# Optimization experiments

Hardware: AMD Instinct MI355X
Metric: run time of the kernel (lower is better)

The kernel has to match this reference:

```python
import jax, jax.numpy as jnp
import numpy as np

# Faithful JAX version of ROIMask_To_Img / paste_mask_in_image (Mask R-CNN paste):
# per box: (mask+1)/2, zero-pad by 1, expand box by (M+2)/M, truncate to int,
# bilinear-resize (align_corners=False, edge-clamped) to the box extent, and
# overwrite-paste into the image canvas; final canvas is mapped to [-1, 1].
# Instead of per-box dynamic-size interpolate + slice assignment, we evaluate the
# bilinear resample densely over the full image grid and mask to the box region
# (same math, jit-compatible, single fused gather-resize-scatter).


def _edge_coords(s, size):
    # torch bilinear align_corners=False with edge clamping
    s = jnp.clip(s, 0.0, size - 1.0)
    i0 = jnp.floor(s)
    t = s - i0
    i0 = i0.astype(jnp.int32)
    i1 = jnp.minimum(i0 + 1, size - 1)
    return i0, i1, t


def _paste_step(im, mask, box):
    # im: [H, W] canvas; mask: [M, M] in [-1,1]; box: [4] float (x0, y0, x1, y1)
    H, W = im.shape
    M = mask.shape[-1]
    Mp = M + 2  # padded mask size
    m = jnp.pad((mask + 1.0) * 0.5, 1)  # expand_masks(padding=1) -> [Mp, Mp]
    scale = (M + 2.0) / M
    w_half = (box[2] - box[0]) * (0.5 * scale)
    h_half = (box[3] - box[1]) * (0.5 * scale)
    x_c = (box[2] + box[0]) * 0.5
    y_c = (box[3] + box[1]) * 0.5
    # expand_boxes then .to(int32) (truncation toward zero, like torch)
    b = jnp.trunc(jnp.stack([x_c - w_half, y_c - h_half,
                             x_c + w_half, y_c + h_half])).astype(jnp.int32)
    w = jnp.maximum(b[2] - b[0] + 1, 1).astype(jnp.float32)
    h = jnp.maximum(b[3] - b[1] + 1, 1).astype(jnp.float32)
    px = jnp.arange(H)
    py = jnp.arange(W)
    # source coords in padded-mask space (align_corners=False)
    sx = (px - b[0] + 0.5) * (Mp / w) - 0.5  # [H]
    sy = (py - b[1] + 0.5) * (Mp / h) - 0.5  # [W]
    x0, x1, tx = _edge_coords(sx, Mp)
    y0, y1, ty = _edge_coords(sy, Mp)
    # separable bilinear: mix rows first ([H, Mp]), then columns ([H, W])
    rowmix = m[x0] * (1.0 - tx)[:, None] + m[x1] * tx[:, None]
    val = rowmix[:, y0] * (1.0 - ty)[None, :] + rowmix[:, y1] * ty[None, :]
    # paste region (overwrite semantics, clipped to the image)
    vx = (px >= b[0]) & (px <= b[2])
    vy = (py >= b[1]) & (py <= b[3])
    return jnp.where(vx[:, None] & vy[None, :], val, im)


def setup_inputs() -> dict:
    key = jax.random.key(0)
    B, N, M, H, W = 32, 16, 28, 1024, 1024
    k1, k2, k3, k4 = jax.random.split(key, 4)
    masks = jax.random.uniform(k1, (B, N, 1, M, M), jnp.float32, -1.0, 1.0)
    # valid boxes inside the image: corner + extent
    p0 = jax.random.uniform(k2, (B, N, 2), jnp.float32, 0.0, H - 64.0)
    ext = jax.random.uniform(k3, (B, N, 2), jnp.float32, 16.0, 200.0)
    p1 = jnp.minimum(p0 + ext, H - 2.0)
    rects = jnp.concatenate([p0, p1], axis=-1)  # [B, N, 4] = (x0, y0, x1, y1)
    instance_mask = jnp.zeros((B, 1, H, W), jnp.float32)
    return {"masks": masks, "rects": rects, "instance_mask": instance_mask}


def reference(masks, rects, instance_mask):
    # masks: [B, N, 1, M, M]; rects: [B, N, 4]; instance_mask: [B, 1, H, W]
    H, W = instance_mask.shape[-2], instance_mask.shape[-1]

    def per_image(masks_b, rects_b):
        im0 = jnp.zeros((H, W), jnp.float32)
        def step(im, xs):
            m, bx = xs
            return _paste_step(im, m, bx), None
        im, _ = jax.lax.scan(step, im0, (masks_b[:, 0], rects_b))
        return im

    im = jax.vmap(per_image)(masks, rects)  # [B, H, W]
    return im[:, None, :, :] * 2.0 - 1.0
```

## Files before the change

### kernel.cpp

```cpp
#include <hip/hip_runtime.h>

constexpr int Bc = 32;
constexpr int Nc = 16;
constexpr int Mc = 28;
constexpr int MPc = 30;
constexpr int Hc = 1024;
constexpr int Wc = 1024;

__global__ __launch_bounds__(256)
void paste_masks_kernel(const float* __restrict__ masks,
                        const float* __restrict__ rects,
                        float* __restrict__ out)
{
    const int bid = blockIdx.x;
    const int b   = bid >> 10;
    const int row = bid & (Hc - 1);
    const int tid = threadIdx.x;

    __shared__ int   s_r0[Nc], s_r2[Nc];
    __shared__ int   s_c1[Nc], s_c3[Nc];
    __shared__ float s_sxs[Nc], s_sys[Nc];
    __shared__ int   s_list[Nc];
    __shared__ int   s_cnt;
    __shared__ float s_rowmix[Nc][MPc];

    if (tid < Nc) {
        const float* r = rects + (b * Nc + tid) * 4;
        const float x0 = r[0], y0 = r[1], x1 = r[2], y1 = r[3];
        const float hs = 0.5357142857142857f;
        const float w_half = (x1 - x0) * hs;
        const float h_half = (y1 - y0) * hs;
        const float xc = (x1 + x0) * 0.5f;
        const float yc = (y1 + y0) * 0.5f;
        const int ib0 = (int)truncf(xc - w_half);
        const int ib1 = (int)truncf(yc - h_half);
        const int ib2 = (int)truncf(xc + w_half);
        const int ib3 = (int)truncf(yc + h_half);
        s_r0[tid] = ib0; s_r2[tid] = ib2;
        s_c1[tid] = ib1; s_c3[tid] = ib3;
        const float w = fmaxf((float)(ib2 - ib0 + 1), 1.0f);
        const float h = fmaxf((float)(ib3 - ib1 + 1), 1.0f);
        s_sxs[tid] = (float)MPc / w;
        s_sys[tid] = (float)MPc / h;
    }
    __syncthreads();

    if (tid == 0) {
        int c = 0;
        for (int n = Nc - 1; n >= 0; --n)
            if (row >= s_r0[n] && row <= s_r2[n]) s_list[c++] = n;
        s_cnt = c;
    }
    __syncthreads();
    const int cnt = s_cnt;

    if (cnt > 0) {
        for (int idx = tid; idx < cnt * MPc; idx += 256) {
            const int k = idx / MPc;
            const int j = idx - k * MPc;
            const int n = s_list[k];
            float sx = ((float)(row - s_r0[n]) + 0.5f) * s_sxs[n] - 0.5f;
            sx = fminf(fmaxf(sx, 0.0f), (float)(MPc - 1));
            const int   i0 = (int)floorf(sx);
            const float tx = sx - (float)i0;
            const int   i1 = min(i0 + 1, MPc - 1);
            const float* mp = masks + (size_t)(b * Nc + n) * (Mc * Mc);
            float m0 = 0.0f, m1 = 0.0f;
            if (i0 >= 1 && i0 <= Mc && j >= 1 && j <= Mc)
                m0 = (mp[(i0 - 1) * Mc + (j - 1)] + 1.0f) * 0.5f;
            if (i1 >= 1 && i1 <= Mc && j >= 1 && j <= Mc)
                m1 = (mp[(i1 - 1) * Mc + (j - 1)] + 1.0f) * 0.5f;
            s_rowmix[k][j] = m0 * (1.0f - tx) + m1 * tx;
        }
        __syncthreads();
    }

    const int col0 = tid * 4;
    float4 v;
    float* vp = (float*)&v;
    #pragma unroll
    for (int c = 0; c < 4; ++c) {
        const int col = col0 + c;
        float val = -1.0f;
        for (int k = 0; k < cnt; ++k) {
            const int n = s_list[k];
            if (col >= s_c1[n] && col <= s_c3[n]) {
                float sy = ((float)(col - s_c1[n]) + 0.5f) * s_sys[n] - 0.5f;
                sy = fminf(fmaxf(sy, 0.0f), (float)(MPc - 1));
                const int   j0 = (int)floorf(sy);
                const float ty = sy - (float)j0;
                const int   j1 = min(j0 + 1, MPc - 1);
                const float s = s_rowmix[k][j0] * (1.0f - ty) + s_rowmix[k][j1] * ty;
                val = s * 2.0f - 1.0f;
                break;
            }
        }
        vp[c] = val;
    }

    float4* op = (float4*)(out + (size_t)bid * Wc) + tid;
    *op = v;
}

extern "C" void kernel_launch(void* const* d_in, const int* in_sizes, int n_in,
                              void* d_out, int out_size, void* d_ws, size_t ws_size,
                              hipStream_t stream) {
    const float* masks = (const float*)d_in[0];
    const float* rects = (const float*)d_in[1];
    float* out = (float*)d_out;

    const int grid = Bc * Hc;
    paste_masks_kernel<<<grid, 256, 0, stream>>>(masks, rects, out);
}
```

Baseline: 256.9 us.

## Process 8 rows per block with box bitmasks and direct global bilinear gathers

Each block now covers 8 output rows instead of one. This spreads the per-block rect setup across more output and cuts the grid by 8x. The serial per-row box list and the shared rowmix staging are replaced by per-row and per-column box bitmasks, and the topmost box is found with a count-leading-zeros. The bilinear sample now does four global (cache-served) mask loads per covered pixel instead of two shared reads, trading extra memory gathers for fewer barriers and no serial thread-0 loop.

```diff
diff --git a/kernel.cpp b/kernel.cpp
--- a/kernel.cpp
+++ b/kernel.cpp
@@ -1,28 +1,28 @@
 #include <hip/hip_runtime.h>
 
-constexpr int Bc = 32;
-constexpr int Nc = 16;
-constexpr int Mc = 28;
+constexpr int Bc  = 32;
+constexpr int Nc  = 16;
+constexpr int Mc  = 28;
 constexpr int MPc = 30;
-constexpr int Hc = 1024;
-constexpr int Wc = 1024;
+constexpr int Hc  = 1024;
+constexpr int Wc  = 1024;
+constexpr int ROWS = 8;
 
 __global__ __launch_bounds__(256)
 void paste_masks_kernel(const float* __restrict__ masks,
                         const float* __restrict__ rects,
                         float* __restrict__ out)
 {
-    const int bid = blockIdx.x;
-    const int b   = bid >> 10;
-    const int row = bid & (Hc - 1);
-    const int tid = threadIdx.x;
+    const int tiles_per_img = Hc / ROWS;
+    const int bid  = blockIdx.x;
+    const int b    = bid / tiles_per_img;
+    const int row0 = (bid - b * tiles_per_img) * ROWS;
+    const int tid  = threadIdx.x;
 
-    __shared__ int   s_r0[Nc], s_r2[Nc];
-    __shared__ int   s_c1[Nc], s_c3[Nc];
-    __shared__ float s_sxs[Nc], s_sys[Nc];
-    __shared__ int   s_list[Nc];
-    __shared__ int   s_cnt;
-    __shared__ float s_rowmix[Nc][MPc];
+    __shared__ int      s_r0[Nc], s_r2[Nc];
+    __shared__ int      s_c1[Nc], s_c3[Nc];
+    __shared__ float    s_sxs[Nc], s_sys[Nc];
+    __shared__ unsigned s_rowmask[ROWS];
 
     if (tid < Nc) {
         const float* r = rects + (b * Nc + tid) * 4;
@@ -45,61 +45,72 @@
     }
     __syncthreads();
 
-    if (tid == 0) {
-        int c = 0;
-        for (int n = Nc - 1; n >= 0; --n)
-            if (row >= s_r0[n] && row <= s_r2[n]) s_list[c++] = n;
-        s_cnt = c;
-    }
-    __syncthreads();
-    const int cnt = s_cnt;
-
-    if (cnt > 0) {
-        for (int idx = tid; idx < cnt * MPc; idx += 256) {
-            const int k = idx / MPc;
-            const int j = idx - k * MPc;
-            const int n = s_list[k];
-            float sx = ((float)(row - s_r0[n]) + 0.5f) * s_sxs[n] - 0.5f;
-            sx = fminf(fmaxf(sx, 0.0f), (float)(MPc - 1));
-            const int   i0 = (int)floorf(sx);
-            const float tx = sx - (float)i0;
-            const int   i1 = min(i0 + 1, MPc - 1);
-            const float* mp = masks + (size_t)(b * Nc + n) * (Mc * Mc);
-            float m0 = 0.0f, m1 = 0.0f;
-            if (i0 >= 1 && i0 <= Mc && j >= 1 && j <= Mc)
-                m0 = (mp[(i0 - 1) * Mc + (j - 1)] + 1.0f) * 0.5f;
-            if (i1 >= 1 && i1 <= Mc && j >= 1 && j <= Mc)
-                m1 = (mp[(i1 - 1) * Mc + (j - 1)] + 1.0f) * 0.5f;
-            s_rowmix[k][j] = m0 * (1.0f - tx) + m1 * tx;
-        }
-        __syncthreads();
+    if (tid < ROWS) {
+        const int row = row0 + tid;
+        unsigned m = 0;
+        #pragma unroll
+        for (int n = 0; n < Nc; ++n)
+            if (row >= s_r0[n] && row <= s_r2[n]) m |= (1u << n);
+        s_rowmask[tid] = m;
     }
 
     const int col0 = tid * 4;
-    float4 v;
-    float* vp = (float*)&v;
+    unsigned cmask[4];
     #pragma unroll
     for (int c = 0; c < 4; ++c) {
         const int col = col0 + c;
-        float val = -1.0f;
-        for (int k = 0; k < cnt; ++k) {
-            const int n = s_list[k];
-            if (col >= s_c1[n] && col <= s_c3[n]) {
+        unsigned m = 0;
+        #pragma unroll
+        for (int n = 0; n < Nc; ++n)
+            if (col >= s_c1[n] && col <= s_c3[n]) m |= (1u << n);
+        cmask[c] = m;
+    }
+    __syncthreads();
+
+    const float* mbase = masks + (size_t)b * (Nc * Mc * Mc);
+    float* orow = out + (size_t)b * Hc * Wc + (size_t)row0 * Wc;
+
+    for (int rr = 0; rr < ROWS; ++rr) {
+        const int row = row0 + rr;
+        const unsigned rm = s_rowmask[rr];
+        float4 v;
+        float* vp = (float*)&v;
+        #pragma unroll
+        for (int c = 0; c < 4; ++c) {
+            const unsigned m = cmask[c] & rm;
+            float val = -1.0f;
+            if (m) {
+                const int n = 31 - __clz((int)m);
+                float sx = ((float)(row - s_r0[n]) + 0.5f) * s_sxs[n] - 0.5f;
+                sx = fminf(fmaxf(sx, 0.0f), (float)(MPc - 1));
+                const int   i0 = (int)floorf(sx);
+                const float tx = sx - (float)i0;
+                const int   i1 = min(i0 + 1, MPc - 1);
+
+                const int col = col0 + c;
                 float sy = ((float)(col - s_c1[n]) + 0.5f) * s_sys[n] - 0.5f;
                 sy = fminf(fmaxf(sy, 0.0f), (float)(MPc - 1));
                 const int   j0 = (int)floorf(sy);
                 const float ty = sy - (float)j0;
                 const int   j1 = min(j0 + 1, MPc - 1);
-                const float s = s_rowmix[k][j0] * (1.0f - ty) + s_rowmix[k][j1] * ty;
-                val = s * 2.0f - 1.0f;
-                break;
+
+                const float* mp = mbase + n * (Mc * Mc);
+                const bool iok0 = (i0 >= 1) & (i0 <= Mc);
+                const bool iok1 = (i1 >= 1) & (i1 <= Mc);
+                const bool jok0 = (j0 >= 1) & (j0 <= Mc);
+                const bool jok1 = (j1 >= 1) & (j1 <= Mc);
+                const float m00 = (iok0 & jok0) ? (mp[(i0-1)*Mc + (j0-1)] + 1.0f) * 0.5f : 0.0f;
+                const float m10 = (iok1 & jok0) ? (mp[(i1-1)*Mc + (j0-1)] + 1.0f) * 0.5f : 0.0f;
+                const float m01 = (iok0 & jok1) ? (mp[(i0-1)*Mc + (j1-1)] + 1.0f) * 0.5f : 0.0f;
+                const float m11 = (iok1 & jok1) ? (mp[(i1-1)*Mc + (j1-1)] + 1.0f) * 0.5f : 0.0f;
+                const float a0 = m00 * (1.0f - tx) + m10 * tx;
+                const float a1 = m01 * (1.0f - tx) + m11 * tx;
+                val = (a0 * (1.0f - ty) + a1 * ty) * 2.0f - 1.0f;
             }
+            vp[c] = val;
         }
-        vp[c] = val;
+        *((float4*)(orow + (size_t)rr * Wc) + tid) = v;
     }
-
-    float4* op = (float4*)(out + (size_t)bid * Wc) + tid;
-    *op = v;
 }
 
 extern "C" void kernel_launch(void* const* d_in, const int* in_sizes, int n_in,
@@ -109,6 +120,6 @@
     const float* rects = (const float*)d_in[1];
     float* out = (float*)d_out;
 
-    const int grid = Bc * Hc;
+    const int grid = Bc * (Hc / ROWS);
     paste_masks_kernel<<<grid, 256, 0, stream>>>(masks, rects, out);
 }
```

New measurement: 250.7 us. 2.4% less time.
